# Kernel optimization log

Measured on AMD Instinct MI355X. Metric: run time of the kernel, lower is better.

## Reference

```python
import jax, jax.numpy as jnp
import numpy as np

K = 3  # dcn kernel size
PAD = (K - 1) // 2
GRAD_MUL = 0.1


def _deform_conv(x, offsets, weight):
    """DCNv1 (no modulation), stride 1, padding PAD, deformable_groups=1.
    x: [B,C,H,W]; offsets: [B,2*K*K,H,W] with (y,x) pairs per kernel point;
    weight: [O,C,K,K]. Returns [B,O,H,W].
    """
    B, C, H, W = x.shape
    K2 = K * K
    off = offsets.reshape(B, K2, 2, H, W)
    base = jnp.arange(K, dtype=x.dtype) - PAD            # [-1, 0, 1]
    base_y = jnp.repeat(base, K)                          # y repeated
    base_x = jnp.tile(base, K)                            # x tiled
    # sampling coordinates: p0 + pk + offset  -> [B,K2,H,W]
    py = jnp.arange(H, dtype=x.dtype)[None, None, :, None] + base_y[None, :, None, None] + off[:, :, 0]
    px = jnp.arange(W, dtype=x.dtype)[None, None, None, :] + base_x[None, :, None, None] + off[:, :, 1]
    y0 = jnp.floor(py)
    x0 = jnp.floor(px)
    ly = py - y0
    lx = px - x0
    y0i = y0.astype(jnp.int32)
    x0i = x0.astype(jnp.int32)
    x_flat = x.reshape(B, C, H * W)

    def corner(yy, xx, w):
        valid = (yy >= 0) & (yy < H) & (xx >= 0) & (xx < W)
        idx = jnp.clip(yy, 0, H - 1) * W + jnp.clip(xx, 0, W - 1)  # [B,K2,H,W]
        g = jax.vmap(lambda xf, ix: jnp.take(xf, ix.reshape(-1), axis=1))(x_flat, idx)
        g = g.reshape(B, C, K2, H, W)
        return g * (w * valid.astype(x.dtype))[:, None]

    sampled = (corner(y0i, x0i, (1 - ly) * (1 - lx))
               + corner(y0i, x0i + 1, (1 - ly) * lx)
               + corner(y0i + 1, x0i, ly * (1 - lx))
               + corner(y0i + 1, x0i + 1, ly * lx))  # [B,C,K2,H,W]
    w_r = weight.reshape(weight.shape[0], C, K2)
    return jnp.einsum('bckhw,ock->bohw', sampled, w_r)


def setup_inputs() -> dict:
    key = jax.random.key(0)
    k1, k2, k3 = jax.random.split(key, 3)
    B, C, H, W, O = 4, 256, 64, 64, 256
    x = jax.random.normal(k1, (B, C, H, W), dtype=jnp.float32)
    shape_pred = jax.random.normal(k2, (B, 2 * K * K, H, W), dtype=jnp.float32)
    weight = jax.random.normal(k3, (O, C, K, K), dtype=jnp.float32) * 0.01  # normal_init std=0.01
    return {"x": x, "shape_pred": shape_pred, "weight": weight}


def reference(x, shape_pred, weight):
    base = jnp.arange(K, dtype=x.dtype) - PAD
    # dcn_base_offset: (y,x) pairs per kernel point, flattened -> [2*K*K]
    dcn_base = jnp.stack([jnp.repeat(base, K), jnp.tile(base, K)], axis=1).reshape(-1)
    sp = shape_pred * GRAD_MUL + jax.lax.stop_gradient(shape_pred) * (1.0 - GRAD_MUL)
    dcn_offset = sp - dcn_base[None, :, None, None]
    return jax.nn.relu(_deform_conv(x, dcn_offset, weight))
```

## Files before the change

kernel.cpp:

```cpp
#include <hip/hip_runtime.h>
#include <hip/hip_bf16.h>

#define BB 4
#define CC 256
#define HH 64
#define WW 64
#define OO 256
#define NK2 9
#define HWP (HH*WW)
#define KD (NK2*CC)
#define PART_ELEMS (BB*OO*HWP)
#define XT_BYTES   8388608ull
#define WT_BYTES   1179648ull
#define PART_OFF   (XT_BYTES + WT_BYTES)

typedef __bf16 bf16x8 __attribute__((ext_vector_type(8)));
typedef float f32x4 __attribute__((ext_vector_type(4)));
typedef float f32x8 __attribute__((ext_vector_type(8)));
typedef unsigned short u16x8 __attribute__((ext_vector_type(8)));

static __device__ __forceinline__ float bf2f(unsigned short v) {
  return __uint_as_float(((unsigned)v) << 16);
}
static __device__ __forceinline__ unsigned short f2bf(float f) {
  __hip_bfloat16 h = __float2bfloat16(f);
  return __builtin_bit_cast(unsigned short, h);
}

__global__ void k_xpose(const float* __restrict__ x, unsigned short* __restrict__ xt) {
  __shared__ float tile[32][33];
  int b  = blockIdx.z;
  int c0 = blockIdx.y * 32;
  int p0 = blockIdx.x * 32;
  int tx = threadIdx.x & 31;
  int ty = threadIdx.x >> 5;
  const float* src = x + ((size_t)b * CC + c0) * HWP + p0;
#pragma unroll
  for (int i = 0; i < 4; ++i)
    tile[ty + i * 8][tx] = src[(size_t)(ty + i * 8) * HWP + tx];
  __syncthreads();
  unsigned short* dst = xt + ((size_t)b * HWP + p0) * CC + c0;
#pragma unroll
  for (int i = 0; i < 4; ++i) {
    float v = tile[tx][ty + i * 8];
    dst[(size_t)(ty + i * 8) * CC + tx] = f2bf(v);
  }
}

__global__ void k_wt(const float* __restrict__ w, unsigned short* __restrict__ wt) {
  int i = blockIdx.x * 256 + threadIdx.x;
  if (i >= OO * KD) return;
  int o = i / KD;
  int r = i - o * KD;
  int kpt = r >> 8;
  int c = r & 255;
  wt[i] = f2bf(w[((size_t)o * CC + c) * NK2 + kpt]);
}

template<int KPTN, int NG, int BF16OUT>
__launch_bounds__(512)
__global__ void k_dcn(const unsigned short* __restrict__ xt,
                      const unsigned short* __restrict__ wt,
                      const float* __restrict__ sp,
                      void* __restrict__ dstv) {
  __shared__ __align__(16) unsigned short Alds[128 * 256];

  const int tid = threadIdx.x;
  constexpr int NBLK = NG * BB * (HH / 2);
  const int hw = blockIdx.x;
  const int swz = (hw & 7) * (NBLK / 8) + (hw >> 3);
  const int g = swz % NG;
  const int rest = swz / NG;
  const int y0 = (rest & 31) * 2;
  const int b = rest >> 5;
  const int kpt0 = g * KPTN;

  const int sm = tid >> 2;
  const int t4 = tid & 3;
  const int rr = sm >> 6;
  const int px = sm & 63;
  const int y = y0 + rr;

  const int wv = tid >> 6;
  const int lane = tid & 63;
  const int l15 = lane & 15;
  const int lg = lane >> 4;
  const int obase = wv * 32;

  float offY[KPTN], offX[KPTN];
#pragma unroll
  for (int t = 0; t < KPTN; ++t) {
    offY[t] = sp[((size_t)b * 18 + 2 * (kpt0 + t)) * HWP + y * WW + px];
    offX[t] = sp[((size_t)b * 18 + 2 * (kpt0 + t) + 1) * HWP + y * WW + px];
  }

  f32x4 acc[2][8];
#pragma unroll
  for (int i = 0; i < 2; ++i)
#pragma unroll
    for (int j = 0; j < 8; ++j)
      acc[i][j] = (f32x4){0.f, 0.f, 0.f, 0.f};

  const unsigned short* wbase[2];
#pragma unroll
  for (int fm = 0; fm < 2; ++fm) {
    int o = obase + fm * 16 + l15;
    wbase[fm] = wt + (size_t)o * KD + 8 * lg;
  }

  char* Ab = (char*)Alds;
  const unsigned short* xb = xt + (size_t)b * HWP * CC;

#pragma unroll
  for (int t = 0; t < KPTN; ++t) {
    const int kpt = kpt0 + t;
    {
      float py = (float)y + offY[t];
      float pxx = (float)px + offX[t];
      float fy = floorf(py), fx = floorf(pxx);
      float ly = py - fy, lx = pxx - fx;
      int y0i = (int)fy, x0i = (int)fx;
      int y1i = y0i + 1, x1i = x0i + 1;
      bool vy0 = (y0i >= 0) & (y0i < HH);
      bool vy1 = (y1i >= 0) & (y1i < HH);
      bool vx0 = (x0i >= 0) & (x0i < WW);
      bool vx1 = (x1i >= 0) & (x1i < WW);
      float w00 = (1.f - ly) * (1.f - lx);
      float w01 = (1.f - ly) * lx;
      float w10 = ly * (1.f - lx);
      float w11 = ly * lx;
      w00 = (vy0 && vx0) ? w00 : 0.f;
      w01 = (vy0 && vx1) ? w01 : 0.f;
      w10 = (vy1 && vx0) ? w10 : 0.f;
      w11 = (vy1 && vx1) ? w11 : 0.f;
      int yc0 = min(max(y0i, 0), HH - 1), yc1 = min(max(y1i, 0), HH - 1);
      int xc0 = min(max(x0i, 0), WW - 1), xc1 = min(max(x1i, 0), WW - 1);
      const unsigned short* p00 = xb + (yc0 * WW + xc0) * CC + t4 * 8;
      const unsigned short* p01 = xb + (yc0 * WW + xc1) * CC + t4 * 8;
      const unsigned short* p10 = xb + (yc1 * WW + xc0) * CC + t4 * 8;
      const unsigned short* p11 = xb + (yc1 * WW + xc1) * CC + t4 * 8;
#pragma unroll
      for (int cg = 0; cg < 8; ++cg) {
        u16x8 a00 = *reinterpret_cast<const u16x8*>(p00 + cg * 32);
        u16x8 a01 = *reinterpret_cast<const u16x8*>(p01 + cg * 32);
        u16x8 a10 = *reinterpret_cast<const u16x8*>(p10 + cg * 32);
        u16x8 a11 = *reinterpret_cast<const u16x8*>(p11 + cg * 32);
        u16x8 r;
#pragma unroll
        for (int j = 0; j < 8; ++j) {
          float s = fmaf(w11, bf2f(a11[j]),
                    fmaf(w10, bf2f(a10[j]),
                    fmaf(w01, bf2f(a01[j]), w00 * bf2f(a00[j]))));
          r[j] = f2bf(s);
        }
        unsigned bo = (unsigned)(sm * 512 + cg * 64 + t4 * 16) ^ (unsigned)((sm & 7) << 4);
        *reinterpret_cast<u16x8*>(Ab + bo) = r;
      }
    }
    __syncthreads();

#define LOADK(AF, BF, KK)                                                          \
    {                                                                              \
      _Pragma("unroll")                                                            \
      for (int fm = 0; fm < 2; ++fm)                                               \
        AF[fm] = __builtin_bit_cast(bf16x8,                                        \
            *reinterpret_cast<const u16x8*>(wbase[fm] + (size_t)kpt * CC + (KK) * 32)); \
      _Pragma("unroll")                                                            \
      for (int fn = 0; fn < 8; ++fn) {                                             \
        int mr = fn * 16 + l15;                                                    \
        unsigned bo = (unsigned)(mr * 512 + (KK) * 64 + lg * 16) ^ (unsigned)((mr & 7) << 4); \
        BF[fn] = __builtin_bit_cast(bf16x8, *reinterpret_cast<const u16x8*>(Ab + bo)); \
      }                                                                            \
    }
#define DOMFMA(AF, BF)                                                             \
    {                                                                              \
      _Pragma("unroll")                                                            \
      for (int fm = 0; fm < 2; ++fm)                                               \
        _Pragma("unroll")                                                          \
        for (int fn = 0; fn < 8; ++fn)                                             \
          acc[fm][fn] = __builtin_amdgcn_mfma_f32_16x16x32_bf16(AF[fm], BF[fn], acc[fm][fn], 0, 0, 0); \
    }
    {
      bf16x8 a0[2], a1[2];
      bf16x8 b0[8], b1[8];
      LOADK(a0, b0, 0);
#pragma unroll
      for (int kk = 0; kk < 8; ++kk) {
        if ((kk & 1) == 0) {
          if (kk < 7) LOADK(a1, b1, kk + 1);
          DOMFMA(a0, b0);
        } else {
          if (kk < 7) LOADK(a0, b0, kk + 1);
          DOMFMA(a1, b1);
        }
      }
    }
    __syncthreads();
  }

#pragma unroll
  for (int fm = 0; fm < 2; ++fm) {
#pragma unroll
    for (int fn = 0; fn < 8; ++fn) {
#pragma unroll
      for (int r = 0; r < 4; ++r) {
        int o = obase + fm * 16 + lg * 4 + r;
        int m = fn * 16 + l15;
        int yy = y0 + (m >> 6);
        int xx = m & 63;
        size_t idx = (((size_t)b * OO + o) * HH + yy) * WW + xx;
        float v = acc[fm][fn][r];
        if (BF16OUT) {
          ((unsigned short*)dstv)[(size_t)g * PART_ELEMS + idx] = f2bf(v);
        } else {
          ((float*)dstv)[idx] = fmaxf(v, 0.0f);
        }
      }
    }
  }
}

__global__ void k_reduce(const unsigned short* __restrict__ parts, float* __restrict__ out, int n8) {
  int i = blockIdx.x * 256 + threadIdx.x;
  if (i >= n8) return;
  const u16x8* p0 = (const u16x8*)parts;
  const u16x8* p1 = p0 + (PART_ELEMS / 8);
  const u16x8* p2 = p1 + (PART_ELEMS / 8);
  u16x8 a = p0[i], b = p1[i], c = p2[i];
  f32x8 o;
#pragma unroll
  for (int j = 0; j < 8; ++j)
    o[j] = fmaxf(bf2f(a[j]) + bf2f(b[j]) + bf2f(c[j]), 0.0f);
  *reinterpret_cast<f32x8*>(out + (size_t)i * 8) = o;
}

extern "C" void kernel_launch(void* const* d_in, const int* in_sizes, int n_in,
                              void* d_out, int out_size, void* d_ws, size_t ws_size,
                              hipStream_t stream) {
  const float* x = (const float*)d_in[0];
  const float* sp = (const float*)d_in[1];
  const float* w = (const float*)d_in[2];
  float* out = (float*)d_out;

  unsigned short* xt = (unsigned short*)d_ws;
  unsigned short* wt = (unsigned short*)((char*)d_ws + XT_BYTES);
  unsigned short* parts = (unsigned short*)((char*)d_ws + PART_OFF);

  k_xpose<<<dim3(HWP / 32, CC / 32, BB), 256, 0, stream>>>(x, xt);
  k_wt<<<(OO * KD + 255) / 256, 256, 0, stream>>>(w, wt);

  const size_t need = PART_OFF + 3ull * PART_ELEMS * sizeof(unsigned short);
  if (ws_size >= need) {
    k_dcn<3, 3, 1><<<3 * BB * (HH / 2), 512, 0, stream>>>(xt, wt, sp, parts);
    k_reduce<<<PART_ELEMS / 8 / 256, 256, 0, stream>>>(parts, out, PART_ELEMS / 8);
  } else {
    k_dcn<9, 1, 0><<<BB * (HH / 2), 512, 0, stream>>>(xt, wt, sp, out);
  }
}
```

Before: 68.39 us.

## Retile weight layout per k-slice and widen gather to 8 lanes per pixel

The transposed weight buffer is reordered to [kpt][k-chunk][o][32], so each MFMA A-fragment load for a given k-slice reads a contiguous 16 KB block instead of striding by the full KD row. The bilinear gather now assigns 8 threads per pixel, each loading 16-byte chunks across two rows, instead of 4 threads per pixel. This gives more contiguous 128-byte segments per corner read. It also doubles the offset registers and changes the LDS write pattern, which affects register pressure and the swizzle's bank behaviour.

New measurement: 60.32 us. -11.8%, faster.

```diff
diff --git a/kernel.cpp b/kernel.cpp
--- a/kernel.cpp
+++ b/kernel.cpp
@@ -50,10 +50,13 @@
 __global__ void k_wt(const float* __restrict__ w, unsigned short* __restrict__ wt) {
   int i = blockIdx.x * 256 + threadIdx.x;
   if (i >= OO * KD) return;
-  int o = i / KD;
-  int r = i - o * KD;
-  int kpt = r >> 8;
-  int c = r & 255;
+  int kpt = i >> 16;
+  int rem = i & 65535;
+  int kk = rem >> 13;
+  int rem2 = rem & 8191;
+  int o = rem2 >> 5;
+  int f = rem2 & 31;
+  int c = kk * 32 + f;
   wt[i] = f2bf(w[((size_t)o * CC + c) * NK2 + kpt]);
 }
 
@@ -75,11 +78,8 @@
   const int b = rest >> 5;
   const int kpt0 = g * KPTN;
 
-  const int sm = tid >> 2;
-  const int t4 = tid & 3;
-  const int rr = sm >> 6;
-  const int px = sm & 63;
-  const int y = y0 + rr;
+  const int t8 = tid & 7;
+  const int pxb = tid >> 3;
 
   const int wv = tid >> 6;
   const int lane = tid & 63;
@@ -87,12 +87,14 @@
   const int lg = lane >> 4;
   const int obase = wv * 32;
 
-  float offY[KPTN], offX[KPTN];
-#pragma unroll
-  for (int t = 0; t < KPTN; ++t) {
-    offY[t] = sp[((size_t)b * 18 + 2 * (kpt0 + t)) * HWP + y * WW + px];
-    offX[t] = sp[((size_t)b * 18 + 2 * (kpt0 + t) + 1) * HWP + y * WW + px];
-  }
+  float offY[2][KPTN], offX[2][KPTN];
+#pragma unroll
+  for (int h = 0; h < 2; ++h)
+#pragma unroll
+    for (int t = 0; t < KPTN; ++t) {
+      offY[h][t] = sp[((size_t)b * 18 + 2 * (kpt0 + t)) * HWP + (y0 + h) * WW + pxb];
+      offX[h][t] = sp[((size_t)b * 18 + 2 * (kpt0 + t) + 1) * HWP + (y0 + h) * WW + pxb];
+    }
 
   f32x4 acc[2][8];
 #pragma unroll
@@ -103,10 +105,8 @@
 
   const unsigned short* wbase[2];
 #pragma unroll
-  for (int fm = 0; fm < 2; ++fm) {
-    int o = obase + fm * 16 + l15;
-    wbase[fm] = wt + (size_t)o * KD + 8 * lg;
-  }
+  for (int fm = 0; fm < 2; ++fm)
+    wbase[fm] = wt + (size_t)(obase + fm * 16 + l15) * 32 + lg * 8;
 
   char* Ab = (char*)Alds;
   const unsigned short* xb = xt + (size_t)b * HWP * CC;
@@ -114,9 +114,11 @@
 #pragma unroll
   for (int t = 0; t < KPTN; ++t) {
     const int kpt = kpt0 + t;
-    {
-      float py = (float)y + offY[t];
-      float pxx = (float)px + offX[t];
+#pragma unroll
+    for (int h = 0; h < 2; ++h) {
+      const int pm = h * 64 + pxb;
+      float py = (float)(y0 + h) + offY[h][t];
+      float pxx = (float)pxb + offX[h][t];
       float fy = floorf(py), fx = floorf(pxx);
       float ly = py - fy, lx = pxx - fx;
       int y0i = (int)fy, x0i = (int)fx;
@@ -135,16 +137,16 @@
       w11 = (vy1 && vx1) ? w11 : 0.f;
       int yc0 = min(max(y0i, 0), HH - 1), yc1 = min(max(y1i, 0), HH - 1);
       int xc0 = min(max(x0i, 0), WW - 1), xc1 = min(max(x1i, 0), WW - 1);
-      const unsigned short* p00 = xb + (yc0 * WW + xc0) * CC + t4 * 8;
-      const unsigned short* p01 = xb + (yc0 * WW + xc1) * CC + t4 * 8;
-      const unsigned short* p10 = xb + (yc1 * WW + xc0) * CC + t4 * 8;
-      const unsigned short* p11 = xb + (yc1 * WW + xc1) * CC + t4 * 8;
-#pragma unroll
-      for (int cg = 0; cg < 8; ++cg) {
-        u16x8 a00 = *reinterpret_cast<const u16x8*>(p00 + cg * 32);
-        u16x8 a01 = *reinterpret_cast<const u16x8*>(p01 + cg * 32);
-        u16x8 a10 = *reinterpret_cast<const u16x8*>(p10 + cg * 32);
-        u16x8 a11 = *reinterpret_cast<const u16x8*>(p11 + cg * 32);
+      const unsigned short* p00 = xb + (yc0 * WW + xc0) * CC + t8 * 8;
+      const unsigned short* p01 = xb + (yc0 * WW + xc1) * CC + t8 * 8;
+      const unsigned short* p10 = xb + (yc1 * WW + xc0) * CC + t8 * 8;
+      const unsigned short* p11 = xb + (yc1 * WW + xc1) * CC + t8 * 8;
+#pragma unroll
+      for (int cg = 0; cg < 4; ++cg) {
+        u16x8 a00 = *reinterpret_cast<const u16x8*>(p00 + cg * 64);
+        u16x8 a01 = *reinterpret_cast<const u16x8*>(p01 + cg * 64);
+        u16x8 a10 = *reinterpret_cast<const u16x8*>(p10 + cg * 64);
+        u16x8 a11 = *reinterpret_cast<const u16x8*>(p11 + cg * 64);
         u16x8 r;
 #pragma unroll
         for (int j = 0; j < 8; ++j) {
@@ -153,7 +155,7 @@
                     fmaf(w01, bf2f(a01[j]), w00 * bf2f(a00[j]))));
           r[j] = f2bf(s);
         }
-        unsigned bo = (unsigned)(sm * 512 + cg * 64 + t4 * 16) ^ (unsigned)((sm & 7) << 4);
+        unsigned bo = (unsigned)(pm * 512 + cg * 128 + t8 * 16) ^ (unsigned)((pm & 7) << 4);
         *reinterpret_cast<u16x8*>(Ab + bo) = r;
       }
     }
@@ -164,7 +166,7 @@
       _Pragma("unroll")                                                            \
       for (int fm = 0; fm < 2; ++fm)                                               \
         AF[fm] = __builtin_bit_cast(bf16x8,                                        \
-            *reinterpret_cast<const u16x8*>(wbase[fm] + (size_t)kpt * CC + (KK) * 32)); \
+            *reinterpret_cast<const u16x8*>(wbase[fm] + (size_t)(kpt * 8 + (KK)) * 8192)); \
       _Pragma("unroll")                                                            \
       for (int fn = 0; fn < 8; ++fn) {                                             \
         int mr = fn * 16 + l15;                                                    \
```
